# Optimization experiments

Measured on AMD Instinct MI355X. Metric: run time of the kernel, lower is better.

## Reference

```python
import jax, jax.numpy as jnp
import numpy as np

N, S, C, P, K = 64, 64, 128, 32, 1000   # batch, frames, in_planes, part_num, class_num
HPG = (3 * C) // 16                      # hidden channels per group for part_score mlp = 24
EPS = 1e-5


def setup_inputs() -> dict:
    key = jax.random.key(0)
    ks = jax.random.split(key, 8)
    return {
        "t_f": jax.random.normal(ks[0], (N, S, C, P), jnp.float32),
        "t_s": jax.random.normal(ks[1], (N, S, C, P), jnp.float32),
        "t_l": jax.random.normal(ks[2], (N, S, C, P), jnp.float32),
        # part_score grouped 1x1 convs (groups=P): per-group (out, in)
        "w1": jax.random.normal(ks[3], (P, HPG, 3 * C), jnp.float32) * 0.05,
        "bn1_gamma": jnp.ones((P, HPG), jnp.float32),
        "bn1_beta": jnp.zeros((P, HPG), jnp.float32),
        "w2": jax.random.normal(ks[4], (P, 1, HPG), jnp.float32) * 0.05,
        # decay_channel grouped 1x1 conv: per-group 3C -> C
        "wd": jax.random.normal(ks[5], (P, C, 3 * C), jnp.float32) * 0.05,
        # per-part BatchNorm1d(C) affine params
        "bn_gamma": jnp.ones((P, C), jnp.float32),
        "bn_beta": jnp.zeros((P, C), jnp.float32),
        # fc: (1, C, K) in torch; squeeze leading 1
        "fc": jax.random.normal(ks[6], (C, K), jnp.float32) * 0.05,
    }


def reference(t_f, t_s, t_l, w1, bn1_gamma, bn1_beta, w2, wd, bn_gamma, bn_beta, fc):
    # cat along channel dim then arrange as (n, p, 3c, s) == grouped conv layout
    x = jnp.concatenate([t_f, t_s, t_l], axis=2).transpose(0, 3, 2, 1)  # (n,p,3c,s)

    # --- part_score: grouped 1x1 conv -> BN (batch stats over n,s) -> LeakyReLU -> grouped conv -> sigmoid
    h = jnp.einsum('npis,poi->npos', x, w1)               # (n,p,HPG,s)
    mu = h.mean(axis=(0, 3), keepdims=True)
    var = h.var(axis=(0, 3), keepdims=True)               # biased var (torch training BN)
    h = (h - mu) / jnp.sqrt(var + EPS) * bn1_gamma[None, :, :, None] + bn1_beta[None, :, :, None]
    h = jnp.where(h >= 0, h, 0.01 * h)                    # LeakyReLU(0.01)
    score = jax.nn.sigmoid(jnp.einsum('npis,poi->npos', h, w2))  # (n,p,1,s)

    # --- decay_channel grouped 1x1 conv: 3c -> c per part
    feat = jnp.einsum('npis,poi->npos', x, wd)            # (n,p,c,s)

    # attention-weighted temporal pooling
    wpv = (feat * score).sum(-1) / score.sum(-1)          # (n,p,c)

    # per-part BatchNorm1d over batch dim (training-mode batch stats)
    m = wpv.mean(axis=0)                                  # (p,c)
    v = wpv.var(axis=0)
    part_feature = ((wpv - m) / jnp.sqrt(v + EPS) * bn_gamma + bn_beta).transpose(1, 0, 2)  # (p,n,c)

    part_classification = jnp.einsum('pnc,ck->pnk', part_feature, fc)  # (p,n,K)

    # argmax frame per (n,p) and gather from t_f
    idx = jnp.argmax(score[:, :, 0, :], axis=-1)          # (n,p)
    tfp = t_f.transpose(0, 3, 1, 2)                       # (n,p,s,c)
    selected = jnp.take_along_axis(tfp, idx[:, :, None, None], axis=2)[:, :, 0, :]  # (n,p,c)
    selected_part_feature = selected.transpose(1, 0, 2)   # (p,n,c)

    weighted_part_vector = wpv.transpose(1, 0, 2)         # (p,n,c)
    return part_classification, weighted_part_vector, selected_part_feature
```

## Files before the change

kernel.cpp:

```cpp
#include <hip/hip_runtime.h>
#include <math.h>

#define N 64
#define S 64
#define C 128
#define P 32
#define KCLS 1000
#define HPG 24
#define C3 384
#define NS 4096
#define EPSV 1e-5f

#define WS_H    0
#define WS_W1Z  (WS_H + 2*P*HPG*NS)
#define WS_BNSS (WS_W1Z + 384*8*32*4)
#define WS_Y    (WS_BNSS + P*HPG*2)
#define WS_Z    (WS_Y + P*N*C3)
#define WS_PF   (WS_Z + P*N)
#define WS_SC   (WS_PF + P*C*N)
#define WS_MI   (WS_SC + N*P*S)

__global__ __launch_bounds__(256) void k0w_w1z(
    const float* __restrict__ w1, float* __restrict__ w1z)
{
  int e = blockIdx.x * 256 + threadIdx.x;
  int p = e & 31;
  int og = (e >> 5) & 7;
  int i = e >> 8;
  float4 v;
  v.x = w1[(p * HPG + og * 3 + 0) * C3 + i];
  v.y = w1[(p * HPG + og * 3 + 1) * C3 + i];
  v.z = w1[(p * HPG + og * 3 + 2) * C3 + i];
  v.w = 0.f;
  ((float4*)w1z)[e] = v;
}

__global__ __launch_bounds__(256) void k01_h(
    const float* __restrict__ tf, const float* __restrict__ ts,
    const float* __restrict__ tl, const float* __restrict__ w1z,
    float* __restrict__ h)
{
  int n = blockIdx.x, st = blockIdx.y, split = blockIdx.z;
  int s0 = st * 8;
  int t = threadIdx.x;
  int p = t & 31;
  int og = t >> 5;
  __shared__ float xl[8 * 1024];
  float acc[3][8];
  #pragma unroll
  for (int oo = 0; oo < 3; ++oo)
    #pragma unroll
    for (int s = 0; s < 8; ++s) acc[oo][s] = 0.f;

  const float4* w4p = (const float4*)w1z;
  const float* srcs[3] = {tf, ts, tl};
  const float* xp = &xl[p];

  for (int ch = 0; ch < 6; ++ch) {
    int gch = split * 6 + ch;
    int z = gch >> 2, c0 = (gch & 3) * 32;
    const float* base = srcs[z] + ((size_t)(n * S + s0)) * C * P + c0 * P;
    if (ch) __syncthreads();
    #pragma unroll
    for (int j = 0; j < 8; ++j) {
      int e = t + 256 * j;
      int s_loc = e >> 8;
      int idx = e & 255;
      float4 v = *(const float4*)&base[(size_t)s_loc * C * P + idx * 4];
      *(float4*)&xl[s_loc * 1024 + idx * 4] = v;
    }
    __syncthreads();
    #pragma unroll 4
    for (int cl = 0; cl < 32; ++cl) {
      int i = gch * 32 + cl;
      float4 w = w4p[(i * 8 + og) * 32 + p];
      float xs[8];
      #pragma unroll
      for (int s = 0; s < 8; ++s) xs[s] = xp[s * 1024 + cl * 32];
      #pragma unroll
      for (int s = 0; s < 8; ++s) {
        acc[0][s] += w.x * xs[s];
        acc[1][s] += w.y * xs[s];
        acc[2][s] += w.z * xs[s];
      }
    }
  }
  #pragma unroll
  for (int oo = 0; oo < 3; ++oo) {
    int o = og * 3 + oo;
    float* hp = h + ((size_t)split * P * HPG + p * HPG + o) * NS + n * S + s0;
    *(float4*)&hp[0] = make_float4(acc[oo][0], acc[oo][1], acc[oo][2], acc[oo][3]);
    *(float4*)&hp[4] = make_float4(acc[oo][4], acc[oo][5], acc[oo][6], acc[oo][7]);
  }
}

__global__ __launch_bounds__(256) void k2_bnstat(const float* __restrict__ h,
    const float* __restrict__ g, const float* __restrict__ b,
    float* __restrict__ bnss)
{
  int po = blockIdx.x;
  int t = threadIdx.x;
  const float4* r0 = (const float4*)(h + (size_t)po * NS);
  const float4* r1 = (const float4*)(h + (size_t)(P * HPG + po) * NS);
  float sm = 0.f, sq = 0.f;
  #pragma unroll
  for (int k = 0; k < 4; ++k) {
    float4 a = r0[t + 256 * k];
    float4 c = r1[t + 256 * k];
    float v0 = a.x + c.x, v1 = a.y + c.y, v2 = a.z + c.z, v3 = a.w + c.w;
    sm += v0 + v1 + v2 + v3;
    sq += v0 * v0 + v1 * v1 + v2 * v2 + v3 * v3;
  }
  #pragma unroll
  for (int m = 1; m < 64; m <<= 1) {
    sm += __shfl_xor(sm, m, 64);
    sq += __shfl_xor(sq, m, 64);
  }
  __shared__ float red[4][2];
  int w = t >> 6;
  if ((t & 63) == 0) { red[w][0] = sm; red[w][1] = sq; }
  __syncthreads();
  if (t == 0) {
    float sum = red[0][0] + red[1][0] + red[2][0] + red[3][0];
    float ssq = red[0][1] + red[1][1] + red[2][1] + red[3][1];
    float mu  = sum / (float)NS;
    float var = ssq / (float)NS - mu * mu;
    float sc = g[po] * rsqrtf(var + EPSV);
    bnss[po * 2]     = sc;
    bnss[po * 2 + 1] = b[po] - mu * sc;
  }
}

__global__ __launch_bounds__(256) void k3a_score(
    const float* __restrict__ h, const float* __restrict__ bnss,
    const float* __restrict__ w2,
    float* __restrict__ score, float* __restrict__ z,
    int* __restrict__ mi_out)
{
  int n = blockIdx.x;
  int p = blockIdx.y * 4 + (threadIdx.x >> 6);
  int l = threadIdx.x & 63;
  float ssum = 0.f;
  const float* hp0 = h + (size_t)p * HPG * NS + n * S;
  const float* hp1 = hp0 + (size_t)P * HPG * NS;
  #pragma unroll
  for (int o = 0; o < HPG; ++o) {
    float hv = hp0[(size_t)o * NS + l] + hp1[(size_t)o * NS + l];
    float sc = bnss[(p * HPG + o) * 2];
    float sh = bnss[(p * HPG + o) * 2 + 1];
    float v = hv * sc + sh;
    v = (v >= 0.f) ? v : 0.01f * v;
    ssum += w2[p * HPG + o] * v;
  }
  float scr = 1.f / (1.f + expf(-ssum));
  float zs = scr;
  #pragma unroll
  for (int m = 1; m < 64; m <<= 1) zs += __shfl_xor(zs, m, 64);
  float mv = scr; int mi = l;
  #pragma unroll
  for (int m = 1; m < 64; m <<= 1) {
    float ov = __shfl_xor(mv, m, 64);
    int   oi = __shfl_xor(mi, m, 64);
    if (ov > mv || (ov == mv && oi < mi)) { mv = ov; mi = oi; }
  }
  if (l == 0) { z[p * N + n] = zs; mi_out[n * P + p] = mi; }
  score[((size_t)n * P + p) * S + l] = scr;
}

__global__ __launch_bounds__(256) void k3b_y(
    const float* __restrict__ tf, const float* __restrict__ ts,
    const float* __restrict__ tl, const float* __restrict__ score,
    const int* __restrict__ mi, float* __restrict__ y,
    float* __restrict__ out_spf)
{
  int n = blockIdx.x, chunk = blockIdx.y;
  int z = chunk >> 2, c0 = (chunk & 3) * 32;
  const float* src = (z == 0) ? tf : (z == 1) ? ts : tl;
  int t = threadIdx.x;
  int p = t & 31, cl = t >> 5;
  __shared__ float sc_lds[S * P];
  __shared__ int mi_lds[P];
  #pragma unroll
  for (int j = 0; j < 8; ++j) {
    int e = t + 256 * j;
    int s2 = e >> 5, pp = e & 31;
    sc_lds[s2 * P + pp] = score[((size_t)n * P + pp) * S + s2];
  }
  if (t < P) mi_lds[t] = mi[n * P + t];
  __syncthreads();
  int mymi = mi_lds[p];
  const float* base = src + (size_t)n * S * C * P + (size_t)(c0 + cl) * P + p;
  float acc[4] = {0.f, 0.f, 0.f, 0.f};
  float sel[4] = {0.f, 0.f, 0.f, 0.f};
  #pragma unroll 8
  for (int s = 0; s < S; ++s) {
    float scv = sc_lds[s * P + p];
    #pragma unroll
    for (int j = 0; j < 4; ++j) {
      float v = base[(size_t)s * C * P + j * 8 * P];
      acc[j] += v * scv;
      sel[j] = (s == mymi) ? v : sel[j];
    }
  }
  float* yp = y + ((size_t)p * N + n) * C3 + z * C + c0 + cl;
  #pragma unroll
  for (int j = 0; j < 4; ++j) yp[j * 8] = acc[j];
  if (z == 0) {
    float* sp = out_spf + ((size_t)p * N + n) * C + c0 + cl;
    #pragma unroll
    for (int j = 0; j < 4; ++j) sp[j * 8] = sel[j];
  }
}

__global__ __launch_bounds__(256) void k4_wpv(
    const float* __restrict__ y, const float* __restrict__ z,
    const float* __restrict__ wd, const float* __restrict__ g,
    const float* __restrict__ b, float* __restrict__ out_wpv,
    float* __restrict__ pf)
{
  int p   = blockIdx.x;
  int cch = blockIdx.y;
  int t = threadIdx.x;
  int n = t & 63, cg = t >> 6;
  int cbase = cch * 16 + cg * 4;
  __shared__ float ych[96][66];
  float acc[4] = {0.f, 0.f, 0.f, 0.f};
  const float* yp  = y  + (size_t)p * N * C3;
  const float* wdp = wd + (size_t)p * C * C3;
  for (int ch = 0; ch < 4; ++ch) {
    __syncthreads();
    #pragma unroll
    for (int j = 0; j < 24; ++j) {
      int e = t + 256 * j;
      int i = e % 96, nn = e / 96;
      ych[i][nn] = yp[nn * C3 + ch * 96 + i];
    }
    __syncthreads();
    #pragma unroll
    for (int sub = 0; sub < 4; ++sub) {
      float yr[24];
      #pragma unroll
      for (int kk = 0; kk < 24; ++kk) yr[kk] = ych[sub * 24 + kk][n];
      int ibase = ch * 96 + sub * 24;
      #pragma unroll
      for (int cl = 0; cl < 4; ++cl) {
        const float4* w4 = (const float4*)(wdp + (size_t)(cbase + cl) * C3 + ibase);
        float a = 0.f;
        #pragma unroll
        for (int q = 0; q < 6; ++q) {
          float4 wv = w4[q];
          a += yr[q*4+0] * wv.x + yr[q*4+1] * wv.y
             + yr[q*4+2] * wv.z + yr[q*4+3] * wv.w;
        }
        acc[cl] += a;
      }
    }
  }
  float zinv = 1.f / z[p * N + n];
  #pragma unroll
  for (int cl = 0; cl < 4; ++cl) acc[cl] *= zinv;
  #pragma unroll
  for (int cl = 0; cl < 4; ++cl) {
    float v = acc[cl];
    float s = v, q = v * v;
    #pragma unroll
    for (int m = 1; m < 64; m <<= 1) {
      s += __shfl_xor(s, m, 64);
      q += __shfl_xor(q, m, 64);
    }
    float mu  = s * (1.f / 64.f);
    float var = q * (1.f / 64.f) - mu * mu;
    int c = cbase + cl;
    float sc = g[p * C + c] * rsqrtf(var + EPSV);
    float sh = b[p * C + c] - mu * sc;
    pf[((size_t)p * C + c) * N + n] = v * sc + sh;
  }
  float4 wout = make_float4(acc[0], acc[1], acc[2], acc[3]);
  *(float4*)(out_wpv + ((size_t)p * N + n) * C + cbase) = wout;
}

__global__ __launch_bounds__(256) void k5_fc(
    const float* __restrict__ pf, const float* __restrict__ fc,
    float* __restrict__ out0)
{
  int kt = blockIdx.x;
  int p  = blockIdx.y;
  int n0 = blockIdx.z * 16;
  int t = threadIdx.x;
  int k = kt * 256 + t;
  bool ok = k < KCLS;
  int kk = ok ? k : (KCLS - 1);
  float acc[16];
  #pragma unroll
  for (int j = 0; j < 16; ++j) acc[j] = 0.f;
  for (int c = 0; c < C; ++c) {
    float fv = fc[c * KCLS + kk];
    const float4* row4 = (const float4*)(pf + ((size_t)p * C + c) * N + n0);
    #pragma unroll
    for (int j4 = 0; j4 < 4; ++j4) {
      float4 r = row4[j4];
      acc[j4*4+0] += r.x * fv; acc[j4*4+1] += r.y * fv;
      acc[j4*4+2] += r.z * fv; acc[j4*4+3] += r.w * fv;
    }
  }
  if (ok) {
    #pragma unroll 4
    for (int j = 0; j < 16; ++j)
      out0[(size_t)(p * N + n0 + j) * KCLS + k] = acc[j];
  }
}

extern "C" void kernel_launch(void* const* d_in, const int* in_sizes, int n_in,
                              void* d_out, int out_size, void* d_ws, size_t ws_size,
                              hipStream_t stream)
{
  const float* tf = (const float*)d_in[0];
  const float* ts = (const float*)d_in[1];
  const float* tl = (const float*)d_in[2];
  const float* w1 = (const float*)d_in[3];
  const float* g1 = (const float*)d_in[4];
  const float* b1 = (const float*)d_in[5];
  const float* w2 = (const float*)d_in[6];
  const float* wd = (const float*)d_in[7];
  const float* g  = (const float*)d_in[8];
  const float* b  = (const float*)d_in[9];
  const float* fc = (const float*)d_in[10];

  float* ws   = (float*)d_ws;
  float* h    = ws + WS_H;
  float* w1z  = ws + WS_W1Z;
  float* bnss = ws + WS_BNSS;
  float* y    = ws + WS_Y;
  float* z    = ws + WS_Z;
  float* pf   = ws + WS_PF;
  float* sc   = ws + WS_SC;
  int*   mi   = (int*)(ws + WS_MI);

  float* out0 = (float*)d_out;
  float* out1 = out0 + P * N * KCLS;
  float* out2 = out1 + P * N * C;

  k0w_w1z<<<384, 256, 0, stream>>>(w1, w1z);
  k01_h<<<dim3(64, 8, 2), 256, 0, stream>>>(tf, ts, tl, w1z, h);
  k2_bnstat<<<768, 256, 0, stream>>>(h, g1, b1, bnss);
  k3a_score<<<dim3(64, 8), 256, 0, stream>>>(h, bnss, w2, sc, z, mi);
  k3b_y<<<dim3(64, 12), 256, 0, stream>>>(tf, ts, tl, sc, mi, y, out2);
  k4_wpv<<<dim3(32, 8), 256, 0, stream>>>(y, z, wd, g, b, out1, pf);
  k5_fc<<<dim3(4, 32, 4), 256, 0, stream>>>(pf, fc, out0);
}
```

Baseline: 163.1 us.

## Double per-thread output channels in h kernel and rotate shared layout

The grouped 1x1 conv kernel for part_score now uses 128 threads per block, with each thread computing 6 output channels instead of 3. This halves the number of shared-memory x loads per FMA and drops the wasted zero lane in the float4 weight packing, which is now three float2 loads. The shared tile is re-laid out as [c][s][p] with a per-channel rotation of the p index to spread accesses across banks. The trade-off is more accumulator registers per thread and half as many threads per block.

```diff
diff --git a/kernel.cpp b/kernel.cpp
--- a/kernel.cpp
+++ b/kernel.cpp
@@ -25,17 +25,18 @@
 {
   int e = blockIdx.x * 256 + threadIdx.x;
   int p = e & 31;
-  int og = (e >> 5) & 7;
-  int i = e >> 8;
-  float4 v;
-  v.x = w1[(p * HPG + og * 3 + 0) * C3 + i];
-  v.y = w1[(p * HPG + og * 3 + 1) * C3 + i];
-  v.z = w1[(p * HPG + og * 3 + 2) * C3 + i];
-  v.w = 0.f;
-  ((float4*)w1z)[e] = v;
-}
-
-__global__ __launch_bounds__(256) void k01_h(
+  int r = e >> 5;
+  int j = r % 3;
+  int r2 = r / 3;
+  int og = r2 & 3;
+  int i = r2 >> 2;
+  float2 v;
+  v.x = w1[(p * HPG + og * 6 + j * 2 + 0) * C3 + i];
+  v.y = w1[(p * HPG + og * 6 + j * 2 + 1) * C3 + i];
+  ((float2*)w1z)[e] = v;
+}
+
+__global__ __launch_bounds__(128) void k01_h(
     const float* __restrict__ tf, const float* __restrict__ ts,
     const float* __restrict__ tl, const float* __restrict__ w1z,
     float* __restrict__ h)
@@ -45,16 +46,15 @@
   int t = threadIdx.x;
   int p = t & 31;
   int og = t >> 5;
-  __shared__ float xl[8 * 1024];
-  float acc[3][8];
-  #pragma unroll
-  for (int oo = 0; oo < 3; ++oo)
+  __shared__ float xl[8192];
+  float acc[6][8];
+  #pragma unroll
+  for (int oo = 0; oo < 6; ++oo)
     #pragma unroll
     for (int s = 0; s < 8; ++s) acc[oo][s] = 0.f;
 
-  const float4* w4p = (const float4*)w1z;
+  const float2* w2p = (const float2*)w1z;
   const float* srcs[3] = {tf, ts, tl};
-  const float* xp = &xl[p];
 
   for (int ch = 0; ch < 6; ++ch) {
     int gch = split * 6 + ch;
@@ -62,32 +62,42 @@
     const float* base = srcs[z] + ((size_t)(n * S + s0)) * C * P + c0 * P;
     if (ch) __syncthreads();
     #pragma unroll
-    for (int j = 0; j < 8; ++j) {
-      int e = t + 256 * j;
+    for (int j = 0; j < 16; ++j) {
+      int e = t + 128 * j;
       int s_loc = e >> 8;
       int idx = e & 255;
+      int c = idx >> 3, p0 = (idx & 7) * 4;
       float4 v = *(const float4*)&base[(size_t)s_loc * C * P + idx * 4];
-      *(float4*)&xl[s_loc * 1024 + idx * 4] = v;
+      int p0r = (p0 + 4 * c) & 31;
+      *(float4*)&xl[c * 256 + s_loc * 32 + p0r] = v;
     }
     __syncthreads();
     #pragma unroll 4
     for (int cl = 0; cl < 32; ++cl) {
       int i = gch * 32 + cl;
-      float4 w = w4p[(i * 8 + og) * 32 + p];
+      int prot = (p + 4 * cl) & 31;
+      const float* xr = &xl[cl * 256 + prot];
       float xs[8];
       #pragma unroll
-      for (int s = 0; s < 8; ++s) xs[s] = xp[s * 1024 + cl * 32];
+      for (int ss = 0; ss < 8; ++ss) xs[ss] = xr[ss * 32];
+      int wb = ((i * 4 + og) * 3) * 32 + p;
+      float2 wa = w2p[wb];
+      float2 wbv = w2p[wb + 32];
+      float2 wc = w2p[wb + 64];
       #pragma unroll
-      for (int s = 0; s < 8; ++s) {
-        acc[0][s] += w.x * xs[s];
-        acc[1][s] += w.y * xs[s];
-        acc[2][s] += w.z * xs[s];
+      for (int ss = 0; ss < 8; ++ss) {
+        acc[0][ss] += wa.x  * xs[ss];
+        acc[1][ss] += wa.y  * xs[ss];
+        acc[2][ss] += wbv.x * xs[ss];
+        acc[3][ss] += wbv.y * xs[ss];
+        acc[4][ss] += wc.x  * xs[ss];
+        acc[5][ss] += wc.y  * xs[ss];
       }
     }
   }
   #pragma unroll
-  for (int oo = 0; oo < 3; ++oo) {
-    int o = og * 3 + oo;
+  for (int oo = 0; oo < 6; ++oo) {
+    int o = og * 6 + oo;
     float* hp = h + ((size_t)split * P * HPG + p * HPG + o) * NS + n * S + s0;
     *(float4*)&hp[0] = make_float4(acc[oo][0], acc[oo][1], acc[oo][2], acc[oo][3]);
     *(float4*)&hp[4] = make_float4(acc[oo][4], acc[oo][5], acc[oo][6], acc[oo][7]);
@@ -340,8 +350,8 @@
   float* out1 = out0 + P * N * KCLS;
   float* out2 = out1 + P * N * C;
 
-  k0w_w1z<<<384, 256, 0, stream>>>(w1, w1z);
-  k01_h<<<dim3(64, 8, 2), 256, 0, stream>>>(tf, ts, tl, w1z, h);
+  k0w_w1z<<<576, 256, 0, stream>>>(w1, w1z);
+  k01_h<<<dim3(64, 8, 2), 128, 0, stream>>>(tf, ts, tl, w1z, h);
   k2_bnstat<<<768, 256, 0, stream>>>(h, g1, b1, bnss);
   k3a_score<<<dim3(64, 8), 256, 0, stream>>>(h, bnss, w2, sc, z, mi);
   k3b_y<<<dim3(64, 12), 256, 0, stream>>>(tf, ts, tl, sc, mi, y, out2);
```

New measurement: 174.3 us. 1.07x slower.

## Remove split-K in h kernel and transpose LDS tile for float4 reads

Applied to the files above, without the earlier changes.

The first-conv kernel no longer splits the 384 input channels across two blocks, so each block accumulates all 12 chunks and writes a single h buffer. The downstream BN-stat and score kernels stop reading and summing two partial buffers. The LDS tile is relaid as [c][s-half][p][4 s] so each thread reads two float4 per channel instead of eight scalars. In exchange, the global loads become scalar strided gathers instead of float4 loads, and the grid has half as many blocks, which may reduce occupancy and latency hiding.

```diff
diff --git a/kernel.cpp b/kernel.cpp
--- a/kernel.cpp
+++ b/kernel.cpp
@@ -25,12 +25,12 @@
 {
   int e = blockIdx.x * 256 + threadIdx.x;
   int p = e & 31;
-  int og = (e >> 5) & 7;
+  int oq = (e >> 5) & 7;
   int i = e >> 8;
   float4 v;
-  v.x = w1[(p * HPG + og * 3 + 0) * C3 + i];
-  v.y = w1[(p * HPG + og * 3 + 1) * C3 + i];
-  v.z = w1[(p * HPG + og * 3 + 2) * C3 + i];
+  v.x = w1[(p * HPG + oq * 3 + 0) * C3 + i];
+  v.y = w1[(p * HPG + oq * 3 + 1) * C3 + i];
+  v.z = w1[(p * HPG + oq * 3 + 2) * C3 + i];
   v.w = 0.f;
   ((float4*)w1z)[e] = v;
 }
@@ -40,12 +40,12 @@
     const float* __restrict__ tl, const float* __restrict__ w1z,
     float* __restrict__ h)
 {
-  int n = blockIdx.x, st = blockIdx.y, split = blockIdx.z;
+  int n = blockIdx.x, st = blockIdx.y;
   int s0 = st * 8;
   int t = threadIdx.x;
   int p = t & 31;
-  int og = t >> 5;
-  __shared__ float xl[8 * 1024];
+  int oq = t >> 5;
+  __shared__ float xl[8192];
   float acc[3][8];
   #pragma unroll
   for (int oo = 0; oo < 3; ++oo)
@@ -54,41 +54,50 @@
 
   const float4* w4p = (const float4*)w1z;
   const float* srcs[3] = {tf, ts, tl};
-  const float* xp = &xl[p];
-
-  for (int ch = 0; ch < 6; ++ch) {
-    int gch = split * 6 + ch;
-    int z = gch >> 2, c0 = (gch & 3) * 32;
-    const float* base = srcs[z] + ((size_t)(n * S + s0)) * C * P + c0 * P;
+
+  for (int ch = 0; ch < 12; ++ch) {
+    int z = ch >> 2, c0 = (ch & 3) * 32;
+    const float* tb = srcs[z] + ((size_t)(n * S + s0)) * C * P + c0 * P;
     if (ch) __syncthreads();
     #pragma unroll
     for (int j = 0; j < 8; ++j) {
-      int e = t + 256 * j;
-      int s_loc = e >> 8;
-      int idx = e & 255;
-      float4 v = *(const float4*)&base[(size_t)s_loc * C * P + idx * 4];
-      *(float4*)&xl[s_loc * 1024 + idx * 4] = v;
+      int a = (t + 256 * j) * 4;
+      int c  = a >> 8;
+      int sh = (a >> 7) & 1;
+      int pp = (a >> 2) & 31;
+      const float* g = tb + (size_t)(sh * 4) * C * P + c * P + pp;
+      float4 v;
+      v.x = g[0];
+      v.y = g[(size_t)1 * C * P];
+      v.z = g[(size_t)2 * C * P];
+      v.w = g[(size_t)3 * C * P];
+      *(float4*)&xl[a] = v;
     }
     __syncthreads();
     #pragma unroll 4
     for (int cl = 0; cl < 32; ++cl) {
-      int i = gch * 32 + cl;
-      float4 w = w4p[(i * 8 + og) * 32 + p];
-      float xs[8];
-      #pragma unroll
-      for (int s = 0; s < 8; ++s) xs[s] = xp[s * 1024 + cl * 32];
-      #pragma unroll
-      for (int s = 0; s < 8; ++s) {
-        acc[0][s] += w.x * xs[s];
-        acc[1][s] += w.y * xs[s];
-        acc[2][s] += w.z * xs[s];
-      }
+      int i = ch * 32 + cl;
+      float4 w  = w4p[(i * 8 + oq) * 32 + p];
+      float4 x0 = *(const float4*)&xl[cl * 256 + p * 4];
+      float4 x1 = *(const float4*)&xl[cl * 256 + 128 + p * 4];
+      acc[0][0] += w.x * x0.x; acc[0][1] += w.x * x0.y;
+      acc[0][2] += w.x * x0.z; acc[0][3] += w.x * x0.w;
+      acc[0][4] += w.x * x1.x; acc[0][5] += w.x * x1.y;
+      acc[0][6] += w.x * x1.z; acc[0][7] += w.x * x1.w;
+      acc[1][0] += w.y * x0.x; acc[1][1] += w.y * x0.y;
+      acc[1][2] += w.y * x0.z; acc[1][3] += w.y * x0.w;
+      acc[1][4] += w.y * x1.x; acc[1][5] += w.y * x1.y;
+      acc[1][6] += w.y * x1.z; acc[1][7] += w.y * x1.w;
+      acc[2][0] += w.z * x0.x; acc[2][1] += w.z * x0.y;
+      acc[2][2] += w.z * x0.z; acc[2][3] += w.z * x0.w;
+      acc[2][4] += w.z * x1.x; acc[2][5] += w.z * x1.y;
+      acc[2][6] += w.z * x1.z; acc[2][7] += w.z * x1.w;
     }
   }
   #pragma unroll
   for (int oo = 0; oo < 3; ++oo) {
-    int o = og * 3 + oo;
-    float* hp = h + ((size_t)split * P * HPG + p * HPG + o) * NS + n * S + s0;
+    int o = oq * 3 + oo;
+    float* hp = h + (size_t)(p * HPG + o) * NS + n * S + s0;
     *(float4*)&hp[0] = make_float4(acc[oo][0], acc[oo][1], acc[oo][2], acc[oo][3]);
     *(float4*)&hp[4] = make_float4(acc[oo][4], acc[oo][5], acc[oo][6], acc[oo][7]);
   }
@@ -101,15 +110,12 @@
   int po = blockIdx.x;
   int t = threadIdx.x;
   const float4* r0 = (const float4*)(h + (size_t)po * NS);
-  const float4* r1 = (const float4*)(h + (size_t)(P * HPG + po) * NS);
   float sm = 0.f, sq = 0.f;
   #pragma unroll
   for (int k = 0; k < 4; ++k) {
     float4 a = r0[t + 256 * k];
-    float4 c = r1[t + 256 * k];
-    float v0 = a.x + c.x, v1 = a.y + c.y, v2 = a.z + c.z, v3 = a.w + c.w;
-    sm += v0 + v1 + v2 + v3;
-    sq += v0 * v0 + v1 * v1 + v2 * v2 + v3 * v3;
+    sm += a.x + a.y + a.z + a.w;
+    sq += a.x * a.x + a.y * a.y + a.z * a.z + a.w * a.w;
   }
   #pragma unroll
   for (int m = 1; m < 64; m <<= 1) {
@@ -141,11 +147,10 @@
   int p = blockIdx.y * 4 + (threadIdx.x >> 6);
   int l = threadIdx.x & 63;
   float ssum = 0.f;
-  const float* hp0 = h + (size_t)p * HPG * NS + n * S;
-  const float* hp1 = hp0 + (size_t)P * HPG * NS;
+  const float* hp = h + (size_t)p * HPG * NS + n * S;
   #pragma unroll
   for (int o = 0; o < HPG; ++o) {
-    float hv = hp0[(size_t)o * NS + l] + hp1[(size_t)o * NS + l];
+    float hv = hp[(size_t)o * NS + l];
     float sc = bnss[(p * HPG + o) * 2];
     float sh = bnss[(p * HPG + o) * 2 + 1];
     float v = hv * sc + sh;
@@ -341,7 +346,7 @@
   float* out2 = out1 + P * N * C;
 
   k0w_w1z<<<384, 256, 0, stream>>>(w1, w1z);
-  k01_h<<<dim3(64, 8, 2), 256, 0, stream>>>(tf, ts, tl, w1z, h);
+  k01_h<<<dim3(64, 8), 256, 0, stream>>>(tf, ts, tl, w1z, h);
   k2_bnstat<<<768, 256, 0, stream>>>(h, g1, b1, bnss);
   k3a_score<<<dim3(64, 8), 256, 0, stream>>>(h, bnss, w2, sc, z, mi);
   k3b_y<<<dim3(64, 12), 256, 0, stream>>>(tf, ts, tl, sc, mi, y, out2);
```

Measured after the change: 173.5 us. 6.4% more time.
